# Kernel tuning notes

Measured on AMD Instinct MI355X. Metric: run time of the kernel, lower is better.

Reference implementation:

```python
import jax, jax.numpy as jnp
import numpy as np

B, S, H, NH = 2, 2048, 1024, 16
HD = H // NH
DFF = 4 * H
EPS = 1e-6


def layer_norm(x, g, b):
    mu = jnp.mean(x, axis=-1, keepdims=True)
    var = jnp.mean(jnp.square(x - mu), axis=-1, keepdims=True)
    return (x - mu) * jax.lax.rsqrt(var + EPS) * g + b


def setup_inputs() -> dict:
    key = jax.random.key(0)
    ks = jax.random.split(key, 10)
    s = 0.02
    return {
        "x": jax.random.normal(ks[0], (B, S, H), jnp.float32),
        "attention_mask": jnp.triu(jnp.ones((S, S), jnp.bool_), k=1),  # causal: True = masked
        "ln1_g": jnp.ones((H,), jnp.float32),
        "ln1_b": jnp.zeros((H,), jnp.float32),
        "ln2_g": jnp.ones((H,), jnp.float32),
        "ln2_b": jnp.zeros((H,), jnp.float32),
        "qkv_w": jax.random.normal(ks[1], (3 * H, H), jnp.float32) * s,
        "out_w": jax.random.normal(ks[2], (H, H), jnp.float32) * s,
        "fc1_w": jax.random.normal(ks[3], (DFF, H), jnp.float32) * s,
        "fc1_b": jnp.zeros((DFF,), jnp.float32),
        "fc2_w": jax.random.normal(ks[4], (H, DFF), jnp.float32) * s,
        "fc2_b": jnp.zeros((H,), jnp.float32),
    }


def reference(x, attention_mask, ln1_g, ln1_b, ln2_g, ln2_b,
              qkv_w, out_w, fc1_w, fc1_b, fc2_w, fc2_b):
    scale = HD ** -0.5
    # --- attention sub-block (pre-norm) ---
    residual = x
    h = layer_norm(x, ln1_g, ln1_b)
    qkv = h @ qkv_w.T                              # [B,S,3H]
    q, k, v = jnp.split(qkv, 3, axis=-1)
    def heads(t):                                  # [B,S,H] -> [B,NH,S,HD]
        return t.reshape(B, S, NH, HD).transpose(0, 2, 1, 3)
    q, k, v = heads(q), heads(k), heads(v)
    scores = jnp.einsum('bhqd,bhkd->bhqk', q, k) * scale
    scores = jnp.where(attention_mask[None, None, :, :], -jnp.inf, scores)
    attn = jax.nn.softmax(scores, axis=-1)
    attn = jnp.nan_to_num(attn, nan=0.0, posinf=0.0, neginf=0.0)
    ctx = jnp.einsum('bhqk,bhkd->bhqd', attn, v)
    ctx = ctx.transpose(0, 2, 1, 3).reshape(B, S, H)
    x = residual + ctx @ out_w.T
    # --- MLP sub-block (pre-norm) ---
    residual = x
    h = layer_norm(x, ln2_g, ln2_b)
    h = jax.nn.gelu(h @ fc1_w.T + fc1_b, approximate=False)
    x = residual + h @ fc2_w.T + fc2_b
    return x
```

## Files before the change

### kernel.cpp

```cpp
#include <hip/hip_runtime.h>
#include <hip/hip_bf16.h>
#include <math.h>

#define B_   2
#define S_   2048
#define H_   1024
#define NH_  16
#define HD_  64
#define DFF_ 4096
#define ROWS (B_*S_)
#define EPS_ 1e-6f
#define NQT  (S_/64)

typedef __hip_bfloat16 bf16;
typedef __attribute__((ext_vector_type(8))) short s8;
typedef __attribute__((ext_vector_type(4))) float f32x4;

__device__ __forceinline__ bf16 to_bf16(float f) { return __float2bfloat16(f); }

#define GLOAD_LDS16(g, l) __builtin_amdgcn_global_load_lds( \
    (const __attribute__((address_space(1))) void*)(g),     \
    (__attribute__((address_space(3))) void*)(l), 16, 0, 0)

__global__ __launch_bounds__(256) void cast_all(const float* __restrict__ w0,
                                                const float* __restrict__ w1,
                                                const float* __restrict__ w2,
                                                const float* __restrict__ w3,
                                                bf16* __restrict__ o0, bf16* __restrict__ o1,
                                                bf16* __restrict__ o2, bf16* __restrict__ o3) {
    size_t u = (size_t)blockIdx.x * 256 + threadIdx.x;
    const size_t n0 = (size_t)3*H_*H_/8, n1 = (size_t)H_*H_/8, n2 = (size_t)DFF_*H_/8;
    const float* src; bf16* dst; size_t base;
    if (u < n0)              { src = w0; dst = o0; base = u; }
    else if (u < n0+n1)      { src = w1; dst = o1; base = u-n0; }
    else if (u < n0+n1+n2)   { src = w2; dst = o2; base = u-n0-n1; }
    else                     { src = w3; dst = o3; base = u-n0-n1-n2; }
    size_t i = base * 8;
    float4 a = *reinterpret_cast<const float4*>(src + i);
    float4 b = *reinterpret_cast<const float4*>(src + i + 4);
    union { bf16 h[8]; s8 v; } uu;
    uu.h[0]=to_bf16(a.x); uu.h[1]=to_bf16(a.y); uu.h[2]=to_bf16(a.z); uu.h[3]=to_bf16(a.w);
    uu.h[4]=to_bf16(b.x); uu.h[5]=to_bf16(b.y); uu.h[6]=to_bf16(b.z); uu.h[7]=to_bf16(b.w);
    *reinterpret_cast<s8*>(dst + i) = uu.v;
}

__global__ __launch_bounds__(256) void ln_bf16(const float* __restrict__ x,
                                               const float* __restrict__ g,
                                               const float* __restrict__ b,
                                               bf16* __restrict__ y) {
    int row = blockIdx.x;
    int t = threadIdx.x;
    float4 v = reinterpret_cast<const float4*>(x + (size_t)row * H_)[t];
    float s  = v.x + v.y + v.z + v.w;
    float ss = v.x*v.x + v.y*v.y + v.z*v.z + v.w*v.w;
    #pragma unroll
    for (int m = 1; m < 64; m <<= 1) {
        s  += __shfl_xor(s,  m, 64);
        ss += __shfl_xor(ss, m, 64);
    }
    __shared__ float ws_s[4], ws_ss[4];
    int wid = t >> 6;
    if ((t & 63) == 0) { ws_s[wid] = s; ws_ss[wid] = ss; }
    __syncthreads();
    s  = ws_s[0] + ws_s[1] + ws_s[2] + ws_s[3];
    ss = ws_ss[0] + ws_ss[1] + ws_ss[2] + ws_ss[3];
    float mu   = s * (1.0f / H_);
    float var  = ss * (1.0f / H_) - mu * mu;
    float rstd = rsqrtf(var + EPS_);
    float4 gv = reinterpret_cast<const float4*>(g)[t];
    float4 bv = reinterpret_cast<const float4*>(b)[t];
    union { bf16 h[4]; short4 sv; } u;
    u.h[0] = to_bf16((v.x - mu) * rstd * gv.x + bv.x);
    u.h[1] = to_bf16((v.y - mu) * rstd * gv.y + bv.y);
    u.h[2] = to_bf16((v.z - mu) * rstd * gv.z + bv.z);
    u.h[3] = to_bf16((v.w - mu) * rstd * gv.w + bv.w);
    *reinterpret_cast<short4*>(y + (size_t)row * H_ + t * 4) = u.sv;
}

template<int EPI, int TN, int OCC, int DB>
__global__ __launch_bounds__(256, OCC) void gemm_bf16(const bf16* __restrict__ A,
                                                      const bf16* __restrict__ Bw,
                                                      bf16* __restrict__ Cb,
                                                      float* __restrict__ Cf,
                                                      bf16* __restrict__ vT,
                                                      const float* __restrict__ bias,
                                                      const float* __restrict__ res,
                                                      int M, int N, int K, int GX) {
    const int NJ = TN / 32;
    const int LA = 128 * 64, LB = TN * 64;
    __shared__ bf16 As[DB * LA];
    __shared__ bf16 Bs[DB * LB];

    int nwg = gridDim.x;
    int ld  = blockIdx.x;
    int wgid = (ld & 7) * (nwg >> 3) + (ld >> 3);
    int by = wgid / GX, bx = wgid % GX;

    int t = threadIdx.x, l = t & 63, w = t >> 6;
    int lr = l & 15, lg = l >> 4;
    size_t bm = (size_t)by * 128, bn = (size_t)bx * TN;

    int srow = t >> 3;
    int skb  = (t & 7) * 8;
    const bf16* Ag = A  + (bm + srow) * K + skb;
    const bf16* Bg = Bw + (bn + srow) * K + skb;

    int wr = (w >> 1) << 6, wc = (w & 1) * (TN / 2);

    f32x4 acc[4][NJ];
    const f32x4 z4 = {0.f, 0.f, 0.f, 0.f};
    #pragma unroll
    for (int i = 0; i < 4; ++i)
        #pragma unroll
        for (int j = 0; j < NJ; ++j) acc[i][j] = z4;

    auto STAGE = [&](int buf, int k0) {
        const bf16* Ak = Ag + k0;
        const bf16* Bk = Bg + k0;
        bf16* Ad = As + buf * LA + w * 512;
        bf16* Bd = Bs + buf * LB + w * 512;
        #pragma unroll
        for (int c = 0; c < 4; ++c)
            GLOAD_LDS16(Ak + (size_t)c * 32 * K, Ad + c * 2048);
        #pragma unroll
        for (int c = 0; c < NJ; ++c)
            GLOAD_LDS16(Bk + (size_t)c * 32 * K, Bd + c * 2048);
    };

    auto COMPUTE = [&](int buf) {
        const bf16* Ab = As + buf * LA;
        const bf16* Bb = Bs + buf * LB;
        #pragma unroll
        for (int kk = 0; kk < 64; kk += 32) {
            s8 af[4], bfr[NJ];
            #pragma unroll
            for (int i = 0; i < 4; ++i)
                af[i] = *reinterpret_cast<const s8*>(Ab + (wr + i*16 + lr) * 64 + kk + lg * 8);
            #pragma unroll
            for (int j = 0; j < NJ; ++j)
                bfr[j] = *reinterpret_cast<const s8*>(Bb + (wc + j*16 + lr) * 64 + kk + lg * 8);
            #pragma unroll
            for (int i = 0; i < 4; ++i)
                #pragma unroll
                for (int j = 0; j < NJ; ++j)
                    acc[i][j] = __builtin_amdgcn_mfma_f32_16x16x32_bf16(af[i], bfr[j], acc[i][j], 0, 0, 0);
        }
    };

    if (DB == 1) {
        for (int k0 = 0; k0 < K; k0 += 64) {
            STAGE(0, k0);
            asm volatile("s_waitcnt vmcnt(0)" ::: "memory");
            __syncthreads();
            COMPUTE(0);
            __syncthreads();
        }
    } else {
        const int NT = K >> 6;
        STAGE(0, 0);
        asm volatile("s_waitcnt vmcnt(0)" ::: "memory");
        __syncthreads();
        int cur = 0;
        for (int it = 0; it < NT; ++it) {
            if (it + 1 < NT) STAGE(cur ^ 1, (it + 1) << 6);
            COMPUTE(cur);
            asm volatile("s_waitcnt vmcnt(0)" ::: "memory");
            __syncthreads();
            cur ^= 1;
        }
    }

    float bias_v[NJ];
    if (EPI == 2 || EPI == 3) {
        #pragma unroll
        for (int j = 0; j < NJ; ++j) bias_v[j] = bias[bn + wc + j*16 + lr];
    }
    #pragma unroll
    for (int i = 0; i < 4; ++i) {
        #pragma unroll
        for (int q = 0; q < 4; ++q) {
            size_t rg = bm + wr + i*16 + lg*4 + q;
            #pragma unroll
            for (int j = 0; j < NJ; ++j) {
                size_t cg = bn + wc + j*16 + lr;
                float v = acc[i][j][q];
                if (EPI == 0) {
                    if (cg < 2048) {
                        Cb[rg * N + cg] = to_bf16(v);
                    } else {
                        int hd = (int)cg - 2048;
                        int hh = hd >> 6, d = hd & 63;
                        int bb = (int)(rg >> 11), sq = (int)(rg & 2047);
                        vT[(((size_t)(bb * NH_ + hh)) * HD_ + d) * S_ + sq] = to_bf16(v);
                    }
                } else if (EPI == 1) {
                    Cf[rg * N + cg] = v + res[rg * N + cg];
                } else if (EPI == 2) {
                    float u = v + bias_v[j];
                    u = 0.5f * u * (1.0f + erff(u * 0.70710678118654752f));
                    Cb[rg * N + cg] = to_bf16(u);
                } else {
                    Cf[rg * N + cg] = v + bias_v[j] + res[rg * N + cg];
                }
            }
        }
    }
}

#define KVB 128

__device__ __forceinline__ s8 scale_q8(s8 v) {
    union { s8 v; bf16 h[8]; } u; u.v = v;
    #pragma unroll
    for (int e = 0; e < 8; ++e)
        u.h[e] = to_bf16(__bfloat162float(u.h[e]) * 0.125f);
    return u.v;
}

__device__ __forceinline__ void attn_qtile(int qt, int h, int b, int t,
                                           const bf16* __restrict__ qkvb,
                                           const bf16* __restrict__ vT,
                                           bf16* __restrict__ ctx,
                                           bf16* Ks, bf16* Vt, bf16* Pw) {
    int l = t & 63, w = t >> 6, lr = l & 15, lg = l >> 4;
    int qb = qt * 64;

    const bf16* qp = qkvb + ((size_t)(b * S_) + qb + w * 16 + lr) * (3 * H_) + h * HD_;
    s8 qf0 = scale_q8(*reinterpret_cast<const s8*>(qp + lg * 8));
    s8 qf1 = scale_q8(*reinterpret_cast<const s8*>(qp + 32 + lg * 8));

    const f32x4 z4 = {0.f, 0.f, 0.f, 0.f};
    f32x4 oacc[4];
    #pragma unroll
    for (int n = 0; n < 4; ++n) oacc[n] = z4;
    float lsum[4] = {0.f, 0.f, 0.f, 0.f};

    int krow = t >> 1, kcol = (t & 1) * 32;
    int vd   = t >> 2, vk = (t & 3) * 8;
    const bf16* kbase = qkvb + ((size_t)(b * S_) + krow) * (3 * H_) + H_ + h * HD_ + kcol;
    const bf16* vbase = vT + ((size_t)((b * NH_ + h) * HD_) + vd) * S_ + vk;

    int nt = (qt >> 1) + 1;
    s8 k0 = *reinterpret_cast<const s8*>(kbase);
    s8 k1 = *reinterpret_cast<const s8*>(kbase + 8);
    s8 k2 = *reinterpret_cast<const s8*>(kbase + 16);
    s8 k3 = *reinterpret_cast<const s8*>(kbase + 24);
    s8 v0 = *reinterpret_cast<const s8*>(vbase);
    s8 v1 = *reinterpret_cast<const s8*>(vbase + 32);
    s8 v2 = *reinterpret_cast<const s8*>(vbase + 64);
    s8 v3 = *reinterpret_cast<const s8*>(vbase + 96);

    for (int it = 0; it < nt; ++it) {
        int kvb0 = it * KVB;
        __syncthreads();
        *reinterpret_cast<s8*>(&Ks[krow * 72 + kcol])      = k0;
        *reinterpret_cast<s8*>(&Ks[krow * 72 + kcol + 8])  = k1;
        *reinterpret_cast<s8*>(&Ks[krow * 72 + kcol + 16]) = k2;
        *reinterpret_cast<s8*>(&Ks[krow * 72 + kcol + 24]) = k3;
        *reinterpret_cast<s8*>(&Vt[vd * 136 + vk])         = v0;
        *reinterpret_cast<s8*>(&Vt[vd * 136 + vk + 32])    = v1;
        *reinterpret_cast<s8*>(&Vt[vd * 136 + vk + 64])    = v2;
        *reinterpret_cast<s8*>(&Vt[vd * 136 + vk + 96])    = v3;
        int nx = (it + 1 < nt) ? kvb0 + KVB : kvb0;
        const bf16* kn = kbase + (size_t)nx * (3 * H_);
        const bf16* vn = vbase + nx;
        k0 = *reinterpret_cast<const s8*>(kn);
        k1 = *reinterpret_cast<const s8*>(kn + 8);
        k2 = *reinterpret_cast<const s8*>(kn + 16);
        k3 = *reinterpret_cast<const s8*>(kn + 24);
        v0 = *reinterpret_cast<const s8*>(vn);
        v1 = *reinterpret_cast<const s8*>(vn + 32);
        v2 = *reinterpret_cast<const s8*>(vn + 64);
        v3 = *reinterpret_cast<const s8*>(vn + 96);
        __syncthreads();

        f32x4 sa[8];
        __builtin_amdgcn_s_setprio(1);
        #pragma unroll
        for (int n = 0; n < 8; ++n) {
            f32x4 zz = z4;
            s8 kf0 = *reinterpret_cast<const s8*>(&Ks[(n*16 + lr) * 72 + lg * 8]);
            s8 kf1 = *reinterpret_cast<const s8*>(&Ks[(n*16 + lr) * 72 + 32 + lg * 8]);
            zz = __builtin_amdgcn_mfma_f32_16x16x32_bf16(qf0, kf0, zz, 0, 0, 0);
            zz = __builtin_amdgcn_mfma_f32_16x16x32_bf16(qf1, kf1, zz, 0, 0, 0);
            sa[n] = zz;
        }
        __builtin_amdgcn_s_setprio(0);

        bool mask = (kvb0 + KVB > qb);
        #pragma unroll
        for (int q = 0; q < 4; ++q) {
            int qrow = qb + w*16 + lg*4 + q;
            #pragma unroll
            for (int n = 0; n < 8; ++n) {
                float s = sa[n][q];
                if (mask) {
                    int col = kvb0 + n*16 + lr;
                    s = (col <= qrow) ? s : -1e30f;
                }
                float e = __expf(s);
                lsum[q] += e;
                Pw[(lg*4 + q) * 136 + n*16 + lr] = to_bf16(e);
            }
        }
        asm volatile("s_waitcnt lgkmcnt(0)" ::: "memory");
        __builtin_amdgcn_sched_barrier(0);

        __builtin_amdgcn_s_setprio(1);
        #pragma unroll
        for (int ks = 0; ks < 4; ++ks) {
            s8 pf = *reinterpret_cast<const s8*>(&Pw[lr * 136 + ks*32 + lg * 8]);
            #pragma unroll
            for (int n = 0; n < 4; ++n) {
                s8 vf = *reinterpret_cast<const s8*>(&Vt[(n*16 + lr) * 136 + ks*32 + lg * 8]);
                oacc[n] = __builtin_amdgcn_mfma_f32_16x16x32_bf16(pf, vf, oacc[n], 0, 0, 0);
            }
        }
        __builtin_amdgcn_s_setprio(0);
    }

    #pragma unroll
    for (int m = 1; m < 16; m <<= 1) {
        #pragma unroll
        for (int q = 0; q < 4; ++q) lsum[q] += __shfl_xor(lsum[q], m, 64);
    }

    #pragma unroll
    for (int q = 0; q < 4; ++q) {
        float inv = 1.0f / lsum[q];
        size_t row = (size_t)(b * S_) + qb + w * 16 + lg * 4 + q;
        #pragma unroll
        for (int n = 0; n < 4; ++n)
            ctx[row * H_ + h * HD_ + n * 16 + lr] = to_bf16(oacc[n][q] * inv);
    }
}

__global__ __launch_bounds__(256) void attn_mfma(const bf16* __restrict__ qkvb,
                                                 const bf16* __restrict__ vT,
                                                 bf16* __restrict__ ctx) {
    __shared__ bf16 Ks[KVB * 72];
    __shared__ bf16 Vt[64 * 136];
    __shared__ bf16 Pw[4][16 * 136];
    int h = blockIdx.y, b = blockIdx.z, t = threadIdx.x;
    int w = t >> 6;
    attn_qtile(blockIdx.x,           h, b, t, qkvb, vT, ctx, Ks, Vt, Pw[w]);
    attn_qtile(NQT - 1 - blockIdx.x, h, b, t, qkvb, vT, ctx, Ks, Vt, Pw[w]);
}

extern "C" void kernel_launch(void* const* d_in, const int* in_sizes, int n_in,
                              void* d_out, int out_size, void* d_ws, size_t ws_size,
                              hipStream_t stream) {
    const float* x     = (const float*)d_in[0];
    const float* ln1_g = (const float*)d_in[2];
    const float* ln1_b = (const float*)d_in[3];
    const float* ln2_g = (const float*)d_in[4];
    const float* ln2_b = (const float*)d_in[5];
    const float* qkv_w = (const float*)d_in[6];
    const float* out_w = (const float*)d_in[7];
    const float* fc1_w = (const float*)d_in[8];
    const float* fc1_b = (const float*)d_in[9];
    const float* fc2_w = (const float*)d_in[10];
    const float* fc2_b = (const float*)d_in[11];
    float* out = (float*)d_out;

    bf16* w_qkv  = (bf16*)d_ws;
    bf16* w_out  = w_qkv  + (size_t)3*H_*H_;
    bf16* w_fc1  = w_out  + (size_t)H_*H_;
    bf16* w_fc2  = w_fc1  + (size_t)DFF_*H_;
    bf16* h_bf   = w_fc2  + (size_t)H_*DFF_;
    bf16* qkv_bf = h_bf   + (size_t)ROWS*H_;
    bf16* vTb    = qkv_bf + (size_t)ROWS*3*H_;
    bf16* ctx_bf = vTb    + (size_t)B_*NH_*HD_*S_;
    bf16* ff_bf  = ctx_bf + (size_t)ROWS*H_;

    cast_all<<<6144, 256, 0, stream>>>(qkv_w, out_w, fc1_w, fc2_w,
                                       w_qkv, w_out, w_fc1, w_fc2);

    ln_bf16<<<ROWS, 256, 0, stream>>>(x, ln1_g, ln1_b, h_bf);
    gemm_bf16<0,128,2,1><<<32 * 24, 256, 0, stream>>>(h_bf, w_qkv, qkv_bf, nullptr, vTb,
                                                      nullptr, nullptr, ROWS, 3*H_, H_, 24);
    attn_mfma<<<dim3(NQT/2, NH_, B_), 256, 0, stream>>>(qkv_bf, vTb, ctx_bf);
    gemm_bf16<1,64,3,2><<<32 * 16, 256, 0, stream>>>(ctx_bf, w_out, nullptr, out, nullptr,
                                                     nullptr, x, ROWS, H_, H_, 16);
    ln_bf16<<<ROWS, 256, 0, stream>>>(out, ln2_g, ln2_b, h_bf);
    gemm_bf16<2,128,2,1><<<32 * 32, 256, 0, stream>>>(h_bf, w_fc1, ff_bf, nullptr, nullptr,
                                                      fc1_b, nullptr, ROWS, DFF_, H_, 32);
    gemm_bf16<3,64,3,2><<<32 * 16, 256, 0, stream>>>(ff_bf, w_fc2, nullptr, out, nullptr,
                                                     fc2_b, out, ROWS, H_, DFF_, 16);
}
```

Before: 266.1 us.

## Add dedicated 256x256-tile FC1 GEMM kernel with swizzled LDS and 8 waves

Replaces the generic 128x128 FC1 GEMM with a specialized kernel using 256x256 output tiles, 512 threads (8 waves, each owning 128x64), XOR-swizzled LDS layout to avoid bank conflicts, double-buffered global-to-LDS loads with explicit vmcnt waits, and s_setprio around MFMA bursts. The larger tile raises arithmetic intensity and reduces redundant global loads. It trades this for a much larger register and LDS footprint (64 KB LDS per block), and the grid drops to 256 blocks, which may leave CUs underfilled. The generic GEMM staging code is also lightly inlined without behavioral change.

```diff
diff --git a/kernel.cpp b/kernel.cpp
--- a/kernel.cpp
+++ b/kernel.cpp
@@ -100,10 +100,8 @@
     int lr = l & 15, lg = l >> 4;
     size_t bm = (size_t)by * 128, bn = (size_t)bx * TN;
 
-    int srow = t >> 3;
-    int skb  = (t & 7) * 8;
-    const bf16* Ag = A  + (bm + srow) * K + skb;
-    const bf16* Bg = Bw + (bn + srow) * K + skb;
+    const bf16* Ag = A  + (bm + (t >> 3)) * K + (t & 7) * 8;
+    const bf16* Bg = Bw + (bn + (t >> 3)) * K + (t & 7) * 8;
 
     int wr = (w >> 1) << 6, wc = (w & 1) * (TN / 2);
 
@@ -115,16 +113,12 @@
         for (int j = 0; j < NJ; ++j) acc[i][j] = z4;
 
     auto STAGE = [&](int buf, int k0) {
-        const bf16* Ak = Ag + k0;
-        const bf16* Bk = Bg + k0;
-        bf16* Ad = As + buf * LA + w * 512;
-        bf16* Bd = Bs + buf * LB + w * 512;
         #pragma unroll
         for (int c = 0; c < 4; ++c)
-            GLOAD_LDS16(Ak + (size_t)c * 32 * K, Ad + c * 2048);
+            GLOAD_LDS16(Ag + k0 + (size_t)c * 32 * K, As + buf * LA + w * 512 + c * 2048);
         #pragma unroll
         for (int c = 0; c < NJ; ++c)
-            GLOAD_LDS16(Bk + (size_t)c * 32 * K, Bd + c * 2048);
+            GLOAD_LDS16(Bg + k0 + (size_t)c * 32 * K, Bs + buf * LB + w * 512 + c * 2048);
     };
 
     auto COMPUTE = [&](int buf) {
@@ -202,6 +196,108 @@
                 } else {
                     Cf[rg * N + cg] = v + bias_v[j] + res[rg * N + cg];
                 }
+            }
+        }
+    }
+}
+
+__global__ __launch_bounds__(512, 2) void gemm256_fc1(const bf16* __restrict__ A,
+                                                      const bf16* __restrict__ Bw,
+                                                      bf16* __restrict__ C,
+                                                      const float* __restrict__ bias,
+                                                      int M, int N, int K) {
+    __shared__ bf16 As[2][256 * 64];
+    __shared__ bf16 Bs[2][256 * 64];
+
+    int nwg = gridDim.x;
+    int ld  = blockIdx.x;
+    int wgid = (ld & 7) * (nwg >> 3) + (ld >> 3);
+    int GX = N >> 8;
+    int by = wgid / GX, bx = wgid % GX;
+    size_t bm = (size_t)by << 8, bn = (size_t)bx << 8;
+
+    int t = threadIdx.x, l = t & 63, w = t >> 6;
+    int lr = l & 15, lg = l >> 4;
+    int wr2 = w >> 2, wc2 = w & 3;
+    int sx = lr & 7;
+
+    int scol = ((l & 7) ^ (l >> 3)) * 8;
+    const bf16* Ag = A  + (bm + w * 8 + (l >> 3)) * K + scol;
+    const bf16* Bg = Bw + (bn + w * 8 + (l >> 3)) * K + scol;
+
+    f32x4 acc[8][4];
+    const f32x4 z4 = {0.f, 0.f, 0.f, 0.f};
+    #pragma unroll
+    for (int i = 0; i < 8; ++i)
+        #pragma unroll
+        for (int j = 0; j < 4; ++j) acc[i][j] = z4;
+
+    auto STAGE = [&](int buf, int k0) {
+        #pragma unroll
+        for (int s = 0; s < 4; ++s)
+            GLOAD_LDS16(Ag + k0 + (size_t)s * 64 * K, &As[buf][s * 4096 + w * 512]);
+        #pragma unroll
+        for (int s = 0; s < 4; ++s)
+            GLOAD_LDS16(Bg + k0 + (size_t)s * 64 * K, &Bs[buf][s * 4096 + w * 512]);
+    };
+
+    auto PHASE = [&](int buf, int mh, int nh) {
+        s8 af[4][2], bfr[2][2];
+        #pragma unroll
+        for (int m4 = 0; m4 < 4; ++m4) {
+            int R = wr2 * 128 + (mh * 4 + m4) * 16 + lr;
+            #pragma unroll
+            for (int kx = 0; kx < 2; ++kx)
+                af[m4][kx] = *reinterpret_cast<const s8*>(&As[buf][R * 64 + (((kx << 2) + lg) ^ sx) * 8]);
+        }
+        #pragma unroll
+        for (int n2 = 0; n2 < 2; ++n2) {
+            int R = wc2 * 64 + (nh * 2 + n2) * 16 + lr;
+            #pragma unroll
+            for (int kx = 0; kx < 2; ++kx)
+                bfr[n2][kx] = *reinterpret_cast<const s8*>(&Bs[buf][R * 64 + (((kx << 2) + lg) ^ sx) * 8]);
+        }
+        __builtin_amdgcn_s_setprio(1);
+        #pragma unroll
+        for (int kx = 0; kx < 2; ++kx)
+            #pragma unroll
+            for (int m4 = 0; m4 < 4; ++m4)
+                #pragma unroll
+                for (int n2 = 0; n2 < 2; ++n2)
+                    acc[mh*4 + m4][nh*2 + n2] =
+                        __builtin_amdgcn_mfma_f32_16x16x32_bf16(af[m4][kx], bfr[n2][kx],
+                                                                acc[mh*4 + m4][nh*2 + n2], 0, 0, 0);
+        __builtin_amdgcn_s_setprio(0);
+        __builtin_amdgcn_sched_barrier(0);
+    };
+
+    const int NT = K >> 6;
+    STAGE(0, 0);
+    STAGE(1, 64);
+    for (int tt = 0; tt < NT; ++tt) {
+        int buf = tt & 1;
+        if (tt + 1 < NT) { asm volatile("s_waitcnt vmcnt(8)" ::: "memory"); }
+        else             { asm volatile("s_waitcnt vmcnt(0)" ::: "memory"); }
+        __builtin_amdgcn_s_barrier();
+        PHASE(buf, 0, 0); PHASE(buf, 0, 1); PHASE(buf, 1, 0); PHASE(buf, 1, 1);
+        __builtin_amdgcn_s_barrier();
+        if (tt + 2 < NT) STAGE(buf, (tt + 2) << 6);
+    }
+
+    float bv[4];
+    int colb = (int)bn + wc2 * 64;
+    #pragma unroll
+    for (int n = 0; n < 4; ++n) bv[n] = bias[colb + n * 16 + lr];
+    #pragma unroll
+    for (int m = 0; m < 8; ++m) {
+        #pragma unroll
+        for (int q = 0; q < 4; ++q) {
+            size_t rg = bm + wr2 * 128 + m * 16 + lg * 4 + q;
+            #pragma unroll
+            for (int n = 0; n < 4; ++n) {
+                float u = acc[m][n][q] + bv[n];
+                u = 0.5f * u * (1.0f + erff(u * 0.70710678118654752f));
+                C[rg * N + colb + n * 16 + lr] = to_bf16(u);
             }
         }
     }
@@ -383,8 +479,7 @@
     gemm_bf16<1,64,3,2><<<32 * 16, 256, 0, stream>>>(ctx_bf, w_out, nullptr, out, nullptr,
                                                      nullptr, x, ROWS, H_, H_, 16);
     ln_bf16<<<ROWS, 256, 0, stream>>>(out, ln2_g, ln2_b, h_bf);
-    gemm_bf16<2,128,2,1><<<32 * 32, 256, 0, stream>>>(h_bf, w_fc1, ff_bf, nullptr, nullptr,
-                                                      fc1_b, nullptr, ROWS, DFF_, H_, 32);
+    gemm256_fc1<<<256, 512, 0, stream>>>(h_bf, w_fc1, ff_bf, fc1_b, ROWS, DFF_, H_);
     gemm_bf16<3,64,3,2><<<32 * 16, 256, 0, stream>>>(ff_bf, w_fc2, nullptr, out, nullptr,
                                                      fc2_b, out, ROWS, H_, DFF_, 16);
 }
```

Result: faster. 252.5 us (-5.1%).
